# Optimization experiments

Measured on AMD Instinct MI355X. Metric: run time of the kernel, lower is better.

## Reference

```python
import jax, jax.numpy as jnp
import numpy as np

B = 32768
E = 10  # number of motion experts


def _p(k, shape, scale=0.05):
    return jax.random.normal(k, shape, dtype=jnp.float32) * scale


def setup_inputs() -> dict:
    key = jax.random.key(0)
    ks = jax.random.split(key, 24)
    inp = {"input_": jax.random.normal(ks[0], (B, 556), dtype=jnp.float32)}
    # encoder 0: pose 400 -> 512 -> 512
    inp["e0_W0"] = _p(ks[1], (400, 512)); inp["e0_b0"] = jnp.zeros((512,), jnp.float32)
    inp["e0_W1"] = _p(ks[2], (512, 512)); inp["e0_b1"] = jnp.zeros((512,), jnp.float32)
    # encoder 1: goal 78 -> 128 -> 128
    inp["e1_W0"] = _p(ks[3], (78, 128)); inp["e1_b0"] = jnp.zeros((128,), jnp.float32)
    inp["e1_W1"] = _p(ks[4], (128, 128)); inp["e1_b1"] = jnp.zeros((128,), jnp.float32)
    # gating NN (1 expert => plain MLP): 78 -> 512 -> 512 -> 10, softmax
    inp["g_W0"] = _p(ks[5], (78, 512)); inp["g_b0"] = jnp.zeros((512,), jnp.float32)
    inp["g_W1"] = _p(ks[6], (512, 512)); inp["g_b1"] = jnp.zeros((512,), jnp.float32)
    inp["g_W2"] = _p(ks[7], (512, 10)); inp["g_b2"] = jnp.zeros((10,), jnp.float32)
    # motion prediction ComponentNN: 10 experts, 640 -> 512 -> 512 -> 578
    inp["m_W0"] = _p(ks[8], (E, 640, 512)); inp["m_b0"] = jnp.zeros((E, 512), jnp.float32)
    inp["m_W1"] = _p(ks[9], (E, 512, 512)); inp["m_b1"] = jnp.zeros((E, 512), jnp.float32)
    inp["m_W2"] = _p(ks[10], (E, 512, 578)); inp["m_b2"] = jnp.zeros((E, 578), jnp.float32)
    return inp


def _expert_layer(x, w, W, b):
    # sum_e w[b,e] * (x[b] @ W[e] + b[e]); blend outputs (equiv. to blending weights)
    return jnp.einsum('be,bi,eio->bo', w, x, W) + w @ b


def reference(input_, e0_W0, e0_b0, e0_W1, e0_b1, e1_W0, e1_b0, e1_W1, e1_b1,
              g_W0, g_b0, g_W1, g_b1, g_W2, g_b2,
              m_W0, m_b0, m_W1, m_b1, m_W2, m_b2):
    elu = jax.nn.elu
    pose = input_[:, 0:400]
    goal = input_[:, 400:478]
    gate_in = input_[:, 478:556]
    # encoders (dropout inactive at inference)
    h0 = elu(elu(pose @ e0_W0 + e0_b0) @ e0_W1 + e0_b1)   # [B,512]
    h1 = elu(elu(goal @ e1_W0 + e1_b0) @ e1_W1 + e1_b1)   # [B,128]
    # gating: softmax over 10 experts
    g = elu(gate_in @ g_W0 + g_b0)
    g = elu(g @ g_W1 + g_b1)
    w = jax.nn.softmax(g @ g_W2 + g_b2, axis=-1)          # [B,10]
    feat = jnp.concatenate([h0, h1], axis=-1)             # [B,640]
    x = elu(_expert_layer(feat, w, m_W0, m_b0))
    x = elu(_expert_layer(x, w, m_W1, m_b1))
    pred = _expert_layer(x, w, m_W2, m_b2)                # [B,578], linear final
    return pred
```

## Files before the change

### kernel.cpp

```cpp
#include <hip/hip_runtime.h>
#include <math.h>

typedef _Float16 h8 __attribute__((ext_vector_type(8)));
typedef float f4 __attribute__((ext_vector_type(4)));

#define BATCH 32768

__device__ __forceinline__ void gload16(const void* g, void* l) {
  __builtin_amdgcn_global_load_lds(
      (const __attribute__((address_space(1))) unsigned int*)g,
      (__attribute__((address_space(3))) unsigned int*)l, 16, 0, 0);
}

__global__ __launch_bounds__(256) void prep_input_k(const float* __restrict__ in,
    _Float16* __restrict__ pose, _Float16* __restrict__ goal, _Float16* __restrict__ gate)
{
  const int b = blockIdx.x;
  const float* r = in + (size_t)b * 556;
  for (int c = threadIdx.x; c < 448; c += 256) {
    float v = (c < 400) ? r[c] : (c == 400 ? 1.0f : 0.0f);
    pose[(size_t)b * 448 + c] = (_Float16)v;
  }
  if (threadIdx.x < 128) {
    int c = threadIdx.x;
    float v = (c < 78) ? r[400 + c] : (c == 78 ? 1.0f : 0.0f);
    goal[(size_t)b * 128 + c] = (_Float16)v;
    float v2 = (c < 78) ? r[478 + c] : (c == 78 ? 1.0f : 0.0f);
    gate[(size_t)b * 128 + c] = (_Float16)v2;
  }
}

__global__ __launch_bounds__(256) void prep_wt_k(const float* __restrict__ W,
    const float* __restrict__ bias, _Float16* __restrict__ out,
    int K, int N, int Nld, int Kout, int biasCols, int biasLd)
{
  __shared__ float tile[64 * 65];
  const int t = threadIdx.x;
  const int c0 = blockIdx.x * 64;
  const int n0 = blockIdx.y * 64;
  {
    const int nn = t & 63;
    #pragma unroll
    for (int i = 0; i < 16; ++i) {
      int cc = (t >> 6) + i * 4;
      int c = c0 + cc, n = n0 + nn;
      float v = 0.0f;
      if (n < N) {
        if (c < K) v = W[(size_t)c * Nld + n];
        else if (c - K < biasCols) v = bias[(size_t)(c - K) * biasLd + n];
      }
      tile[cc * 65 + nn] = v;
    }
  }
  __syncthreads();
  {
    const int cc = t & 63;
    #pragma unroll
    for (int i = 0; i < 16; ++i) {
      int nn = (t >> 6) + i * 4;
      out[(size_t)(n0 + nn) * Kout + c0 + cc] = (_Float16)tile[cc * 65 + nn];
    }
  }
}

template<bool EPI_BIAS, bool DO_ELU, bool OUT_F32>
__global__ __launch_bounds__(256, 2) void gemm_k(
    const _Float16* __restrict__ A, const _Float16* __restrict__ Bw,
    void* __restrict__ OutP, const float* __restrict__ bias,
    int ldA, int ldB, int ldO, int nChunks, int nLimit)
{
  __shared__ __align__(16) _Float16 As[2][128 * 64];
  __shared__ __align__(16) _Float16 Bs[2][128 * 64];

  const int t = threadIdx.x;
  const int m0 = blockIdx.x * 128;
  const int n0 = blockIdx.y * 128;
  const int wid = t >> 6;
  const int lane = t & 63;
  const int wm = (wid >> 1) * 64;
  const int wn = (wid & 1) * 64;
  const int lr = lane & 15;
  const int lg = lane >> 4;

  const int gr = lane >> 3;
  const int gcol = ((lane & 7) ^ gr) * 8;
  const _Float16* Abase = A + (size_t)(m0 + wid * 32 + gr) * ldA + gcol;
  const _Float16* Bbase = Bw + (size_t)(n0 + wid * 32 + gr) * ldB + gcol;

  f4 acc[4][4];
  #pragma unroll
  for (int i = 0; i < 4; ++i)
    #pragma unroll
    for (int j = 0; j < 4; ++j) { f4 z = {0.f, 0.f, 0.f, 0.f}; acc[i][j] = z; }

  auto issue = [&](int c, int buf) {
    #pragma unroll
    for (int i = 0; i < 4; ++i) {
      gload16(Abase + (size_t)(i * 8) * ldA + c * 64, &As[buf][(wid * 32 + i * 8) * 64]);
      gload16(Bbase + (size_t)(i * 8) * ldB + c * 64, &Bs[buf][(wid * 32 + i * 8) * 64]);
    }
  };

  auto mfma_step = [&](const _Float16* as, const _Float16* bs) {
    #pragma unroll
    for (int kk = 0; kk < 2; ++kk) {
      h8 af[4], bf[4];
      const int kslot = kk * 4 + lg;
      #pragma unroll
      for (int i = 0; i < 4; ++i) {
        const int row = wm + i * 16 + lr;
        af[i] = *reinterpret_cast<const h8*>(&as[row * 64 + ((kslot ^ (row & 7)) << 3)]);
      }
      #pragma unroll
      for (int j = 0; j < 4; ++j) {
        const int row = wn + j * 16 + lr;
        bf[j] = *reinterpret_cast<const h8*>(&bs[row * 64 + ((kslot ^ (row & 7)) << 3)]);
      }
      #pragma unroll
      for (int i = 0; i < 4; ++i)
        #pragma unroll
        for (int j = 0; j < 4; ++j)
          acc[i][j] = __builtin_amdgcn_mfma_f32_16x16x32_f16(af[i], bf[j], acc[i][j], 0, 0, 0);
    }
  };

  issue(0, 0);
  int cur = 0;
  for (int c = 0; c < nChunks; ++c) {
    __syncthreads();
    if (c + 1 < nChunks) issue(c + 1, cur ^ 1);
    mfma_step(As[cur], Bs[cur]);
    cur ^= 1;
  }

  #pragma unroll
  for (int j = 0; j < 4; ++j) {
    const int col = n0 + wn + j * 16 + lr;
    if (col >= nLimit) continue;
    float bvv = 0.0f;
    if (EPI_BIAS) bvv = bias[col];
    #pragma unroll
    for (int i = 0; i < 4; ++i) {
      const int rowb = m0 + wm + i * 16 + lg * 4;
      #pragma unroll
      for (int r = 0; r < 4; ++r) {
        float x = acc[i][j][r] + bvv;
        if (DO_ELU) x = (x > 0.0f) ? x : expm1f(x);
        if (OUT_F32)
          reinterpret_cast<float*>(OutP)[(size_t)(rowb + r) * ldO + col] = x;
        else
          reinterpret_cast<_Float16*>(OutP)[(size_t)(rowb + r) * ldO + col] = (_Float16)x;
      }
    }
  }
}

template<int KCe, bool DO_ELU, bool OUT_F32>
__global__ __launch_bounds__(256, 2) void expertD_k(
    const _Float16* __restrict__ A, const _Float16* __restrict__ Bw,
    void* __restrict__ OutP, const _Float16* __restrict__ wpad,
    int ldA, int ldB, int ldO, int nLimit)
{
  constexpr int E = 10;
  __shared__ __align__(16) _Float16 lds[16384 + 16384 + 2560];
  _Float16* Bs = lds + 16384;
  _Float16* wT = lds + 32768;

  const int tid = threadIdx.x;
  const int w = tid >> 6;
  const int l = tid & 63;
  const int m0 = blockIdx.x * 256;
  const int n0 = blockIdx.y * 128;
  const int lr = l & 15;
  const int lg = l >> 4;

  const int strow = tid >> 3;
  const int scol = ((tid & 7) ^ (strow & 7)) * 8;

  auto stB = [&](int buf, size_t colEl) {
    _Float16* d = Bs + buf * 8192 + w * 512;
    const _Float16* s = Bw + (size_t)(n0 + strow) * ldB + colEl + scol;
    #pragma unroll
    for (int p = 0; p < 4; ++p)
      gload16(s + (size_t)(p * 32) * ldB, d + p * 2048);
  };
  auto stA = [&](const _Float16* base, size_t ld, size_t colEl) {
    _Float16* d = lds + w * 512;
    const _Float16* s = base + (size_t)(m0 + strow) * ld + colEl + scol;
    #pragma unroll
    for (int p = 0; p < 8; ++p)
      gload16(s + (size_t)(p * 32) * ld, d + p * 2048);
  };

  auto frag = [&](const _Float16* base, int row, int kslot) -> h8 {
    return *reinterpret_cast<const h8*>(base + row * 64 + ((kslot ^ (row & 7)) << 3));
  };

  f4 acc[4][8];
  #pragma unroll
  for (int mi = 0; mi < 4; ++mi)
    #pragma unroll
    for (int ni = 0; ni < 8; ++ni) { f4 z = {0.f, 0.f, 0.f, 0.f}; acc[mi][ni] = z; }

  #pragma unroll
  for (int idx = tid; idx < 2560; idx += 256) {
    const int m = idx & 255, e = idx >> 8;
    wT[e * 256 + m] = wpad[(size_t)(m0 + m) * 64 + e];
  }
  stA(A, (size_t)ldA, 0);
  stB(0, 0);
  asm volatile("s_waitcnt vmcnt(0) lgkmcnt(0)" ::: "memory");
  __builtin_amdgcn_s_barrier();
  __builtin_amdgcn_sched_barrier(0);

  int s = 0;
  #pragma unroll 1
  for (int kc = 0; kc < KCe; ++kc) {
    #pragma unroll 1
    for (int e = 0; e < E; ++e, ++s) {
      const _Float16* Bh = Bs + (s & 1) * 8192;

      if (e + 1 < E)         stB((s + 1) & 1, (size_t)((e + 1) * KCe + kc) * 64);
      else if (kc + 1 < KCe) stB((s + 1) & 1, (size_t)(kc + 1) * 64);
      else                   stB((s + 1) & 1, (size_t)(E * KCe) * 64);
      __builtin_amdgcn_sched_barrier(0);

      _Float16 se[4];
      #pragma unroll
      for (int j = 0; j < 4; ++j) se[j] = wT[e * 256 + w * 64 + j * 16 + lr];

      #pragma unroll
      for (int kk = 0; kk < 2; ++kk) {
        h8 bf[8];
        #pragma unroll
        for (int ni = 0; ni < 8; ++ni) bf[ni] = frag(Bh, ni * 16 + lr, kk * 4 + lg);
        h8 aa[4];
        #pragma unroll
        for (int mi = 0; mi < 4; ++mi) {
          h8 v = frag(lds, w * 64 + mi * 16 + lr, kk * 4 + lg);
          const _Float16 sv = se[mi];
          #pragma unroll
          for (int q = 0; q < 8; ++q) v[q] = v[q] * sv;
          aa[mi] = v;
        }
        __builtin_amdgcn_s_setprio(1);
        #pragma unroll
        for (int mi = 0; mi < 4; ++mi)
          #pragma unroll
          for (int ni = 0; ni < 8; ++ni)
            acc[mi][ni] = __builtin_amdgcn_mfma_f32_16x16x32_f16(aa[mi], bf[ni], acc[mi][ni], 0, 0, 0);
        __builtin_amdgcn_s_setprio(0);
      }

      __builtin_amdgcn_sched_barrier(0);
      asm volatile("s_waitcnt vmcnt(0)" ::: "memory");
      __builtin_amdgcn_s_barrier();
      __builtin_amdgcn_sched_barrier(0);
      if (e == E - 1) {
        if (kc + 1 < KCe) stA(A, (size_t)ldA, (size_t)(kc + 1) * 64);
        else              stA(wpad, 64, 0);
        asm volatile("s_waitcnt vmcnt(0)" ::: "memory");
        __builtin_amdgcn_s_barrier();
        __builtin_amdgcn_sched_barrier(0);
      }
    }
  }

  {
    const _Float16* Bh = Bs + (s & 1) * 8192;
    #pragma unroll
    for (int kk = 0; kk < 2; ++kk) {
      h8 bf[8];
      #pragma unroll
      for (int ni = 0; ni < 8; ++ni) bf[ni] = frag(Bh, ni * 16 + lr, kk * 4 + lg);
      h8 aa[4];
      #pragma unroll
      for (int mi = 0; mi < 4; ++mi)
        aa[mi] = frag(lds, w * 64 + mi * 16 + lr, kk * 4 + lg);
      #pragma unroll
      for (int mi = 0; mi < 4; ++mi)
        #pragma unroll
        for (int ni = 0; ni < 8; ++ni)
          acc[mi][ni] = __builtin_amdgcn_mfma_f32_16x16x32_f16(aa[mi], bf[ni], acc[mi][ni], 0, 0, 0);
    }
  }

  #pragma unroll
  for (int ni = 0; ni < 8; ++ni) {
    const int col = n0 + ni * 16 + lr;
    if (col >= nLimit) continue;
    #pragma unroll
    for (int mi = 0; mi < 4; ++mi) {
      const int rowb = m0 + w * 64 + mi * 16 + lg * 4;
      #pragma unroll
      for (int r = 0; r < 4; ++r) {
        float x = acc[mi][ni][r];
        if (DO_ELU) x = (x > 0.0f) ? x : expm1f(x);
        if (OUT_F32)
          reinterpret_cast<float*>(OutP)[(size_t)(rowb + r) * ldO + col] = x;
        else
          reinterpret_cast<_Float16*>(OutP)[(size_t)(rowb + r) * ldO + col] = (_Float16)x;
      }
    }
  }
}

__global__ __launch_bounds__(256) void gate_softmax_k(const _Float16* __restrict__ gb,
    const float* __restrict__ W2, const float* __restrict__ b2, _Float16* __restrict__ wpad)
{
  __shared__ float W2s[5120];
  for (int i = threadIdx.x; i < 5120; i += 256) W2s[i] = W2[i];
  __syncthreads();
  const int t = threadIdx.x;
  const int sub = t & 3;
  const int b = blockIdx.x * 64 + (t >> 2);
  const _Float16* row = gb + (size_t)b * 512 + sub * 128;
  float acc[10];
  #pragma unroll
  for (int o = 0; o < 10; ++o) acc[o] = 0.0f;
  #pragma unroll 4
  for (int k0 = 0; k0 < 128; k0 += 8) {
    h8 x = *reinterpret_cast<const h8*>(row + k0);
    #pragma unroll
    for (int jj = 0; jj < 8; ++jj) {
      float xv = (float)x[jj];
      const int k = sub * 128 + k0 + jj;
      #pragma unroll
      for (int o = 0; o < 10; ++o) acc[o] += xv * W2s[k * 10 + o];
    }
  }
  #pragma unroll
  for (int o = 0; o < 10; ++o) {
    acc[o] += __shfl_xor(acc[o], 1);
    acc[o] += __shfl_xor(acc[o], 2);
    acc[o] += b2[o];
  }
  float mx = acc[0];
  #pragma unroll
  for (int o = 1; o < 10; ++o) mx = fmaxf(mx, acc[o]);
  float s = 0.0f;
  #pragma unroll
  for (int o = 0; o < 10; ++o) { acc[o] = expf(acc[o] - mx); s += acc[o]; }
  const float inv = 1.0f / s;
  h8 o0 = {0,0,0,0,0,0,0,0}, o1 = {0,0,0,0,0,0,0,0};
  if (sub == 0) {
    #pragma unroll
    for (int o = 0; o < 8; ++o) o0[o] = (_Float16)(acc[o] * inv);
    o1[0] = (_Float16)(acc[8] * inv);
    o1[1] = (_Float16)(acc[9] * inv);
  }
  _Float16* wr = wpad + (size_t)b * 64 + sub * 16;
  *reinterpret_cast<h8*>(wr) = o0;
  *reinterpret_cast<h8*>(wr + 8) = o1;
}

extern "C" void kernel_launch(void* const* d_in, const int* in_sizes, int n_in,
                              void* d_out, int out_size, void* d_ws, size_t ws_size,
                              hipStream_t stream)
{
  const float* input_ = (const float*)d_in[0];
  const float* e0_W0 = (const float*)d_in[1];
  const float* e0_b0 = (const float*)d_in[2];
  const float* e0_W1 = (const float*)d_in[3];
  const float* e0_b1 = (const float*)d_in[4];
  const float* e1_W0 = (const float*)d_in[5];
  const float* e1_b0 = (const float*)d_in[6];
  const float* e1_W1 = (const float*)d_in[7];
  const float* e1_b1 = (const float*)d_in[8];
  const float* g_W0  = (const float*)d_in[9];
  const float* g_b0  = (const float*)d_in[10];
  const float* g_W1  = (const float*)d_in[11];
  const float* g_b1  = (const float*)d_in[12];
  const float* g_W2  = (const float*)d_in[13];
  const float* g_b2  = (const float*)d_in[14];
  const float* m_W0  = (const float*)d_in[15];
  const float* m_b0  = (const float*)d_in[16];
  const float* m_W1  = (const float*)d_in[17];
  const float* m_b1  = (const float*)d_in[18];
  const float* m_W2  = (const float*)d_in[19];
  const float* m_b2  = (const float*)d_in[20];
  (void)in_sizes; (void)n_in; (void)out_size; (void)ws_size;

  char* ws = (char*)d_ws;
  size_t off = 0;
  auto alloc = [&](size_t bytes) { char* p = ws + off; off += (bytes + 255) & ~(size_t)255; return p; };

  const size_t Bn = BATCH;
  _Float16* wsA    = (_Float16*)alloc(Bn * 512 * 2);
  _Float16* wsB    = (_Float16*)alloc(Bn * 512 * 2);
  _Float16* wsC    = (_Float16*)alloc(Bn * 640 * 2);
  _Float16* goal16 = (_Float16*)alloc(Bn * 128 * 2);
  _Float16* gate16 = (_Float16*)alloc(Bn * 128 * 2);
  _Float16* h1a16  = (_Float16*)alloc(Bn * 128 * 2);
  _Float16* wpad16 = (_Float16*)alloc(Bn * 64 * 2);
  _Float16* e0W0t  = (_Float16*)alloc((size_t)512 * 448 * 2);
  _Float16* e0W1t  = (_Float16*)alloc((size_t)512 * 512 * 2);
  _Float16* e1W0t  = (_Float16*)alloc((size_t)128 * 128 * 2);
  _Float16* e1W1t  = (_Float16*)alloc((size_t)128 * 128 * 2);
  _Float16* gW0t   = (_Float16*)alloc((size_t)512 * 128 * 2);
  _Float16* gW1t   = (_Float16*)alloc((size_t)512 * 512 * 2);
  _Float16* W0b    = (_Float16*)alloc((size_t)512 * 6464 * 2);
  _Float16* W1b    = (_Float16*)alloc((size_t)512 * 5184 * 2);
  _Float16* W2b    = (_Float16*)alloc((size_t)768 * 5184 * 2);

  dim3 blk(256);
  const int BIG = 1 << 30;

  prep_input_k<<<BATCH, blk, 0, stream>>>(input_, wsA, goal16, gate16);

  prep_wt_k<<<dim3(7, 8),    blk, 0, stream>>>(e0_W0, e0_b0, e0W0t, 400, 512, 512, 448, 1, 0);
  prep_wt_k<<<dim3(8, 8),    blk, 0, stream>>>(e0_W1, nullptr, e0W1t, 512, 512, 512, 512, 0, 0);
  prep_wt_k<<<dim3(2, 2),    blk, 0, stream>>>(e1_W0, e1_b0, e1W0t, 78, 128, 128, 128, 1, 0);
  prep_wt_k<<<dim3(2, 2),    blk, 0, stream>>>(e1_W1, nullptr, e1W1t, 128, 128, 128, 128, 0, 0);
  prep_wt_k<<<dim3(2, 8),    blk, 0, stream>>>(g_W0, g_b0, gW0t, 78, 512, 512, 128, 1, 0);
  prep_wt_k<<<dim3(8, 8),    blk, 0, stream>>>(g_W1, nullptr, gW1t, 512, 512, 512, 512, 0, 0);
  prep_wt_k<<<dim3(101, 8),  blk, 0, stream>>>(m_W0, m_b0, W0b, 6400, 512, 512, 6464, 10, 512);
  prep_wt_k<<<dim3(81, 8),   blk, 0, stream>>>(m_W1, m_b1, W1b, 5120, 512, 512, 5184, 10, 512);
  prep_wt_k<<<dim3(81, 12),  blk, 0, stream>>>(m_W2, m_b2, W2b, 5120, 578, 578, 5184, 10, 578);

  gemm_k<false, true, false><<<dim3(256, 4), blk, 0, stream>>>(
      wsA, e0W0t, wsB, nullptr, 448, 448, 512, 7, BIG);
  gemm_k<true, true, false><<<dim3(256, 4), blk, 0, stream>>>(
      wsB, e0W1t, wsC, e0_b1, 512, 512, 640, 8, BIG);
  gemm_k<false, true, false><<<dim3(256, 1), blk, 0, stream>>>(
      goal16, e1W0t, h1a16, nullptr, 128, 128, 128, 2, BIG);
  gemm_k<true, true, false><<<dim3(256, 1), blk, 0, stream>>>(
      h1a16, e1W1t, wsC + 512, e1_b1, 128, 128, 640, 2, BIG);
  gemm_k<false, true, false><<<dim3(256, 4), blk, 0, stream>>>(
      gate16, gW0t, wsA, nullptr, 128, 128, 512, 2, BIG);
  gemm_k<true, true, false><<<dim3(256, 4), blk, 0, stream>>>(
      wsA, gW1t, wsB, g_b1, 512, 512, 512, 8, BIG);
  gate_softmax_k<<<dim3(BATCH / 64), blk, 0, stream>>>(wsB, g_W2, g_b2, wpad16);

  expertD_k<10, true, false><<<dim3(128, 4), blk, 0, stream>>>(
      wsC, W0b, wsA, wpad16, 640, 6464, 512, BIG);
  expertD_k<8, true, false><<<dim3(128, 4), blk, 0, stream>>>(
      wsA, W1b, wsC, wpad16, 512, 5184, 512, BIG);
  expertD_k<8, false, true><<<dim3(128, 5), blk, 0, stream>>>(
      wsC, W2b, d_out, wpad16, 512, 5184, 578, 578);
}
```

Baseline: 863.5 us.

## Hold expert A-operand tiles in registers and vectorize input prep

The expert kernels now load the activation (A) fragments straight from global memory into registers once per K chunk and reuse them across all 10 experts, instead of staging them through LDS. This removes the extra barrier pass per K chunk and halves LDS use, which could allow more resident blocks. In exchange it costs more registers and uses uncoalesced direct global reads whose latency is not overlapped behind a barrier. The input prep kernel also switches to a grid-stride loop that writes 8 halves per thread.

```diff
diff --git a/kernel.cpp b/kernel.cpp
--- a/kernel.cpp
+++ b/kernel.cpp
@@ -12,21 +12,41 @@
       (__attribute__((address_space(3))) unsigned int*)l, 16, 0, 0);
 }
 
-__global__ __launch_bounds__(256) void prep_input_k(const float* __restrict__ in,
+__global__ __launch_bounds__(256) void prep_input2_k(const float* __restrict__ in,
     _Float16* __restrict__ pose, _Float16* __restrict__ goal, _Float16* __restrict__ gate)
 {
-  const int b = blockIdx.x;
-  const float* r = in + (size_t)b * 556;
-  for (int c = threadIdx.x; c < 448; c += 256) {
-    float v = (c < 400) ? r[c] : (c == 400 ? 1.0f : 0.0f);
-    pose[(size_t)b * 448 + c] = (_Float16)v;
-  }
-  if (threadIdx.x < 128) {
-    int c = threadIdx.x;
-    float v = (c < 78) ? r[400 + c] : (c == 78 ? 1.0f : 0.0f);
-    goal[(size_t)b * 128 + c] = (_Float16)v;
-    float v2 = (c < 78) ? r[478 + c] : (c == 78 ? 1.0f : 0.0f);
-    gate[(size_t)b * 128 + c] = (_Float16)v2;
+  const long long total = (long long)BATCH * 88;
+  for (long long i = (long long)blockIdx.x * 256 + threadIdx.x; i < total;
+       i += (long long)gridDim.x * 256) {
+    const int b = (int)(i / 88);
+    const int g = (int)(i % 88);
+    const float* r = in + (size_t)b * 556;
+    h8 v;
+    if (g < 56) {
+      const int c0 = g * 8;
+      #pragma unroll
+      for (int j = 0; j < 8; ++j) {
+        const int c = c0 + j;
+        v[j] = (_Float16)((c < 400) ? r[c] : (c == 400 ? 1.0f : 0.0f));
+      }
+      *reinterpret_cast<h8*>(pose + (size_t)b * 448 + c0) = v;
+    } else if (g < 72) {
+      const int c0 = (g - 56) * 8;
+      #pragma unroll
+      for (int j = 0; j < 8; ++j) {
+        const int c = c0 + j;
+        v[j] = (_Float16)((c < 78) ? r[400 + c] : (c == 78 ? 1.0f : 0.0f));
+      }
+      *reinterpret_cast<h8*>(goal + (size_t)b * 128 + c0) = v;
+    } else {
+      const int c0 = (g - 72) * 8;
+      #pragma unroll
+      for (int j = 0; j < 8; ++j) {
+        const int c = c0 + j;
+        v[j] = (_Float16)((c < 78) ? r[478 + c] : (c == 78 ? 1.0f : 0.0f));
+      }
+      *reinterpret_cast<h8*>(gate + (size_t)b * 128 + c0) = v;
+    }
   }
 }
 
@@ -156,15 +176,15 @@
 }
 
 template<int KCe, bool DO_ELU, bool OUT_F32>
-__global__ __launch_bounds__(256, 2) void expertD_k(
+__global__ __launch_bounds__(256, 2) void expertR_k(
     const _Float16* __restrict__ A, const _Float16* __restrict__ Bw,
     void* __restrict__ OutP, const _Float16* __restrict__ wpad,
     int ldA, int ldB, int ldO, int nLimit)
 {
   constexpr int E = 10;
-  __shared__ __align__(16) _Float16 lds[16384 + 16384 + 2560];
-  _Float16* Bs = lds + 16384;
-  _Float16* wT = lds + 32768;
+  __shared__ __align__(16) _Float16 lds[16384 + 2560];
+  _Float16* Bs = lds;
+  _Float16* wT = lds + 16384;
 
   const int tid = threadIdx.x;
   const int w = tid >> 6;
@@ -184,18 +204,21 @@
     for (int p = 0; p < 4; ++p)
       gload16(s + (size_t)(p * 32) * ldB, d + p * 2048);
   };
-  auto stA = [&](const _Float16* base, size_t ld, size_t colEl) {
-    _Float16* d = lds + w * 512;
-    const _Float16* s = base + (size_t)(m0 + strow) * ld + colEl + scol;
-    #pragma unroll
-    for (int p = 0; p < 8; ++p)
-      gload16(s + (size_t)(p * 32) * ld, d + p * 2048);
-  };
 
   auto frag = [&](const _Float16* base, int row, int kslot) -> h8 {
     return *reinterpret_cast<const h8*>(base + row * 64 + ((kslot ^ (row & 7)) << 3));
   };
 
+  h8 araw[2][4];
+  auto loadA = [&](const _Float16* base, size_t ld, size_t col0) {
+    #pragma unroll
+    for (int kk = 0; kk < 2; ++kk)
+      #pragma unroll
+      for (int mi = 0; mi < 4; ++mi)
+        araw[kk][mi] = *reinterpret_cast<const h8*>(
+            base + (size_t)(m0 + w * 64 + mi * 16 + lr) * ld + col0 + (size_t)(kk * 4 + lg) * 8);
+  };
+
   f4 acc[4][8];
   #pragma unroll
   for (int mi = 0; mi < 4; ++mi)
@@ -207,7 +230,7 @@
     const int m = idx & 255, e = idx >> 8;
     wT[e * 256 + m] = wpad[(size_t)(m0 + m) * 64 + e];
   }
-  stA(A, (size_t)ldA, 0);
+  loadA(A, (size_t)ldA, 0);
   stB(0, 0);
   asm volatile("s_waitcnt vmcnt(0) lgkmcnt(0)" ::: "memory");
   __builtin_amdgcn_s_barrier();
@@ -237,7 +260,7 @@
         h8 aa[4];
         #pragma unroll
         for (int mi = 0; mi < 4; ++mi) {
-          h8 v = frag(lds, w * 64 + mi * 16 + lr, kk * 4 + lg);
+          h8 v = araw[kk][mi];
           const _Float16 sv = se[mi];
           #pragma unroll
           for (int q = 0; q < 8; ++q) v[q] = v[q] * sv;
@@ -256,14 +279,9 @@
       asm volatile("s_waitcnt vmcnt(0)" ::: "memory");
       __builtin_amdgcn_s_barrier();
       __builtin_amdgcn_sched_barrier(0);
-      if (e == E - 1) {
-        if (kc + 1 < KCe) stA(A, (size_t)ldA, (size_t)(kc + 1) * 64);
-        else              stA(wpad, 64, 0);
-        asm volatile("s_waitcnt vmcnt(0)" ::: "memory");
-        __builtin_amdgcn_s_barrier();
-        __builtin_amdgcn_sched_barrier(0);
-      }
-    }
+    }
+    if (kc + 1 < KCe) loadA(A, (size_t)ldA, (size_t)(kc + 1) * 64);
+    else              loadA(wpad, 64, 0);
   }
 
   {
@@ -273,15 +291,11 @@
       h8 bf[8];
       #pragma unroll
       for (int ni = 0; ni < 8; ++ni) bf[ni] = frag(Bh, ni * 16 + lr, kk * 4 + lg);
-      h8 aa[4];
-      #pragma unroll
-      for (int mi = 0; mi < 4; ++mi)
-        aa[mi] = frag(lds, w * 64 + mi * 16 + lr, kk * 4 + lg);
       #pragma unroll
       for (int mi = 0; mi < 4; ++mi)
         #pragma unroll
         for (int ni = 0; ni < 8; ++ni)
-          acc[mi][ni] = __builtin_amdgcn_mfma_f32_16x16x32_f16(aa[mi], bf[ni], acc[mi][ni], 0, 0, 0);
+          acc[mi][ni] = __builtin_amdgcn_mfma_f32_16x16x32_f16(araw[kk][mi], bf[ni], acc[mi][ni], 0, 0, 0);
     }
   }
 
@@ -406,7 +420,7 @@
   dim3 blk(256);
   const int BIG = 1 << 30;
 
-  prep_input_k<<<BATCH, blk, 0, stream>>>(input_, wsA, goal16, gate16);
+  prep_input2_k<<<dim3(2048), blk, 0, stream>>>(input_, wsA, goal16, gate16);
 
   prep_wt_k<<<dim3(7, 8),    blk, 0, stream>>>(e0_W0, e0_b0, e0W0t, 400, 512, 512, 448, 1, 0);
   prep_wt_k<<<dim3(8, 8),    blk, 0, stream>>>(e0_W1, nullptr, e0W1t, 512, 512, 512, 512, 0, 0);
@@ -432,10 +446,10 @@
       wsA, gW1t, wsB, g_b1, 512, 512, 512, 8, BIG);
   gate_softmax_k<<<dim3(BATCH / 64), blk, 0, stream>>>(wsB, g_W2, g_b2, wpad16);
 
-  expertD_k<10, true, false><<<dim3(128, 4), blk, 0, stream>>>(
+  expertR_k<10, true, false><<<dim3(128, 4), blk, 0, stream>>>(
       wsC, W0b, wsA, wpad16, 640, 6464, 512, BIG);
-  expertD_k<8, true, false><<<dim3(128, 4), blk, 0, stream>>>(
+  expertR_k<8, true, false><<<dim3(128, 4), blk, 0, stream>>>(
       wsA, W1b, wsC, wpad16, 512, 5184, 512, BIG);
-  expertD_k<8, false, true><<<dim3(128, 5), blk, 0, stream>>>(
+  expertR_k<8, false, true><<<dim3(128, 5), blk, 0, stream>>>(
       wsC, W2b, d_out, wpad16, 512, 5184, 578, 578);
 }
```

Result: no change. 870.2 us (+0.8%).
